# Performance work log

Measured on AMD Instinct MI355X. Metric: run time of the kernel, lower is better.

Reference implementation:

```python
import jax, jax.numpy as jnp
import numpy as np

B, S, D, H = 4, 4096, 1024, 64

def setup_inputs() -> dict:
    key = jax.random.key(0)
    k1, k2, k3, k4 = jax.random.split(key, 4)
    inp = {
        'input': jax.random.normal(k1, (B, S, D), dtype=jnp.float32),
        'Wq': jax.random.normal(k2, (D, H), dtype=jnp.float32) * (D ** -0.5),
        'Wk': jax.random.normal(k3, (D, H), dtype=jnp.float32) * (D ** -0.5),
        'Wv': jax.random.normal(k4, (D, H), dtype=jnp.float32) * (D ** -0.5),
    }
    return inp

def reference(input, Wq, Wk, Wv):
    # Projections: [B,S,D] @ [D,H] -> [B,S,H]
    q = input @ Wq
    k = input @ Wk
    v = input @ Wv
    head_size = Wq.shape[-1]
    # Scaled scores: [B,S,S]
    scores = jnp.einsum('bqh,bkh->bqk', q, k) * (head_size ** -0.5)
    seq_len = input.shape[1]
    causal = jnp.tril(jnp.ones((seq_len, seq_len), dtype=bool))
    masked = jnp.where(causal, scores, -jnp.inf)
    weights = jax.nn.softmax(masked, axis=-1)
    # dropout p=0.0 -> identity
    return jnp.einsum('bqk,bkh->bqh', weights, v)
```

## Files before the change

kernel.cpp:

```cpp
#include <hip/hip_runtime.h>

#define NS 8

typedef __attribute__((ext_vector_type(8))) short sh8;
typedef __attribute__((ext_vector_type(4))) short sh4;
typedef __attribute__((ext_vector_type(4))) float f4;

#define QSCALE 0.18033688011112042f

typedef const __attribute__((address_space(1))) unsigned int* gas_t;
typedef __attribute__((address_space(3))) unsigned int* las_t;
#define GLD16(g, l) __builtin_amdgcn_global_load_lds((gas_t)(g), (las_t)(l), 16, 0, 0)

static __device__ __forceinline__ unsigned short f2bf(float f) {
  unsigned u = __builtin_bit_cast(unsigned, f);
  u += 0x7fffu + ((u >> 16) & 1u);
  return (unsigned short)(u >> 16);
}
static __device__ __forceinline__ float bf2f(unsigned short s) {
  unsigned u = ((unsigned)s) << 16;
  return __builtin_bit_cast(float, u);
}

__global__ __launch_bounds__(256) void wt_kernel(const float* __restrict__ Wq,
                                                 const float* __restrict__ Wk,
                                                 const float* __restrict__ Wv,
                                                 unsigned short* __restrict__ Wt) {
  __shared__ float tile[64 * 65];
  int widx = blockIdx.x >> 4, kt = blockIdx.x & 15;
  const float* W = widx == 0 ? Wq : (widx == 1 ? Wk : Wv);
  int t = threadIdx.x;
  {
    int kl = t >> 2, seg = (t & 3) * 16;
    const float* src = W + (size_t)(kt * 64 + kl) * 64 + seg;
#pragma unroll
    for (int j = 0; j < 16; ++j) tile[kl * 65 + seg + j] = src[j];
  }
  __syncthreads();
  {
    int nl = t >> 2, ks = (t & 3) * 16;
    unsigned short* dst = Wt + (size_t)(widx * 64 + nl) * 1024 + kt * 64 + ks;
#pragma unroll
    for (int j = 0; j < 16; ++j) dst[j] = f2bf(tile[(ks + j) * 65 + nl]);
  }
}

__global__ __launch_bounds__(256, 4) void proj_kernel(const float* __restrict__ in,
                                                      const unsigned short* __restrict__ Wt,
                                                      unsigned short* __restrict__ Qg,
                                                      unsigned short* __restrict__ Kg,
                                                      unsigned short* __restrict__ Vtg) {
  __shared__ __align__(16) char lds[32768];
  int t = threadIdx.x;
  int w = t >> 6, lane = t & 63, q = lane >> 4, l15 = lane & 15;
  int m0 = blockIdx.x * 32;

  int mt_s = w >> 1, i_s = w & 1;
  const float* ga = in + (size_t)(m0 + mt_s * 16 + l15) * 1024 + q * 8 + i_s * 4;
  const unsigned short* gb = Wt + (size_t)(w * 48 + l15) * 1024 + q * 8;

  f4 acc[2][3];
  f4 z = {0.f, 0.f, 0.f, 0.f};
#pragma unroll
  for (int mt = 0; mt < 2; ++mt)
#pragma unroll
    for (int nt = 0; nt < 3; ++nt) acc[mt][nt] = z;

#define STAGE(kt, buf)                                                        \
  {                                                                           \
    int k0 = (kt) * 32;                                                       \
    char* base = lds + (buf) * 16384;                                         \
    GLD16(ga + k0, base + w * 1024);                                          \
    GLD16(gb + k0, base + 4096 + (w * 3 + 0) * 1024);                         \
    GLD16(gb + 16384 + k0, base + 4096 + (w * 3 + 1) * 1024);                 \
    GLD16(gb + 32768 + k0, base + 4096 + (w * 3 + 2) * 1024);                 \
  }

  STAGE(0, 0);
  for (int kt = 0; kt < 32; ++kt) {
    int cur = kt & 1;
    __syncthreads();
    if (kt + 1 < 32) STAGE(kt + 1, cur ^ 1);

    const f4* Af = (const f4*)(lds + cur * 16384);
    f4 lo0 = Af[0 * 64 + lane], hi0 = Af[1 * 64 + lane];
    f4 lo1 = Af[2 * 64 + lane], hi1 = Af[3 * 64 + lane];
    sh8 a0, a1;
#pragma unroll
    for (int j = 0; j < 4; ++j) {
      a0[j] = (short)f2bf(lo0[j]); a0[4 + j] = (short)f2bf(hi0[j]);
      a1[j] = (short)f2bf(lo1[j]); a1[4 + j] = (short)f2bf(hi1[j]);
    }
    const sh8* Bf = (const sh8*)(lds + cur * 16384 + 4096);
#pragma unroll
    for (int nt = 0; nt < 3; ++nt) {
      sh8 bf = Bf[(w * 3 + nt) * 64 + lane];
      acc[0][nt] = __builtin_amdgcn_mfma_f32_16x16x32_bf16(a0, bf, acc[0][nt], 0, 0, 0);
      acc[1][nt] = __builtin_amdgcn_mfma_f32_16x16x32_bf16(a1, bf, acc[1][nt], 0, 0, 0);
    }
  }
#undef STAGE

  float* vred = (float*)lds;
#pragma unroll
  for (int nt = 0; nt < 3; ++nt) {
    int band = w * 3 + nt;
#pragma unroll
    for (int mt = 0; mt < 2; ++mt)
#pragma unroll
      for (int r = 0; r < 4; ++r) {
        int row = mt * 16 + q * 4 + r;
        float v = acc[mt][nt][r];
        if (band < 4) {
          Qg[(size_t)(m0 + row) * 64 + band * 16 + l15] = f2bf(v * QSCALE);
        } else if (band < 8) {
          Kg[(size_t)(m0 + row) * 64 + (band - 4) * 16 + l15] = f2bf(v);
        } else {
          vred[row * 69 + (band - 8) * 16 + l15] = v;
        }
      }
  }
  __syncthreads();
  {
    int h = t >> 2, sl = (t & 3) * 8;
    int bb = m0 >> 12, s0 = m0 & 4095;
    sh8 vv;
#pragma unroll
    for (int j = 0; j < 8; ++j) vv[j] = (short)f2bf(vred[(sl + j) * 69 + h]);
    *(sh8*)&Vtg[(((size_t)(bb * 64 + h)) << 12) + s0 + sl] = vv;
  }
}

__global__ __launch_bounds__(256, 4) void attn_split(const unsigned short* __restrict__ Qg,
                                                     const unsigned short* __restrict__ Kg,
                                                     const unsigned short* __restrict__ Vtg,
                                                     unsigned short* __restrict__ Opart,
                                                     float* __restrict__ Lpart) {
  __shared__ unsigned short Ks[64 * 72];
  __shared__ unsigned short Vs[64 * 72];
  __shared__ unsigned short Pw[4 * 16 * 72];
  int t = threadIdx.x;
  int b = blockIdx.y;
  int qt = 63 - (int)(blockIdx.x >> 3);
  int sp = blockIdx.x & 7;
  int wave = t >> 6, lane = t & 63, quad = lane >> 4, l15 = lane & 15;
  unsigned short* Pws = Pw + wave * 16 * 72;

  int qrow0 = qt * 64 + wave * 16;
  size_t pbase = ((size_t)sp * 4 + b) * 4096;

  int nkt = qt + 1;
  int chunk = (nkt + NS - 1) / NS;
  int t0 = sp * chunk, t1 = min(nkt, t0 + chunk);
  if (t0 >= t1) {
#pragma unroll
    for (int r = 0; r < 4; ++r) {
      size_t row = pbase + qrow0 + quad * 4 + r;
#pragma unroll
      for (int ht = 0; ht < 4; ++ht) Opart[row * 64 + ht * 16 + l15] = 0;
      if (l15 == 0) Lpart[row] = 0.f;
    }
    return;
  }

  sh8 qa[2];
#pragma unroll
  for (int ks = 0; ks < 2; ++ks)
    qa[ks] = *(const sh8*)&Qg[(size_t)((b << 12) + qrow0 + l15) * 64 + ks * 32 + quad * 8];

  sh8 ones;
#pragma unroll
  for (int j = 0; j < 8; ++j) ones[j] = (short)0x3F80;

  f4 o[5];
  f4 z = {0.f, 0.f, 0.f, 0.f};
#pragma unroll
  for (int ht = 0; ht < 5; ++ht) o[ht] = z;

  int r0 = t >> 3, o0 = (t & 7) * 8;
  int r1 = (t + 256) >> 3, o1 = ((t + 256) & 7) * 8;
  const unsigned short* kg0 = Kg + (size_t)((b << 12) + r0) * 64 + o0;
  const unsigned short* kg1 = Kg + (size_t)((b << 12) + r1) * 64 + o1;
  const unsigned short* vg0 = Vtg + (((size_t)(b * 64 + r0)) << 12) + o0;
  const unsigned short* vg1 = Vtg + (((size_t)(b * 64 + r1)) << 12) + o1;

  sh8 kr0, kr1, vr0, vr1;
  {
    size_t ko = (size_t)t0 * 64 * 64;
    kr0 = *(const sh8*)(kg0 + ko); kr1 = *(const sh8*)(kg1 + ko);
    vr0 = *(const sh8*)(vg0 + t0 * 64); vr1 = *(const sh8*)(vg1 + t0 * 64);
  }

  for (int kt = t0; kt < t1; ++kt) {
    __syncthreads();
    *(sh8*)&Ks[r0 * 72 + o0] = kr0;
    *(sh8*)&Ks[r1 * 72 + o1] = kr1;
    *(sh8*)&Vs[r0 * 72 + o0] = vr0;
    *(sh8*)&Vs[r1 * 72 + o1] = vr1;
    if (kt + 1 < t1) {
      size_t ko = (size_t)(kt + 1) * 64 * 64;
      kr0 = *(const sh8*)(kg0 + ko); kr1 = *(const sh8*)(kg1 + ko);
      vr0 = *(const sh8*)(vg0 + (kt + 1) * 64); vr1 = *(const sh8*)(vg1 + (kt + 1) * 64);
    }
    __syncthreads();

    f4 st[4];
#pragma unroll
    for (int nt = 0; nt < 4; ++nt) st[nt] = z;
#pragma unroll
    for (int ks = 0; ks < 2; ++ks) {
#pragma unroll
      for (int nt = 0; nt < 4; ++nt) {
        sh8 kb = *(const sh8*)&Ks[(nt * 16 + l15) * 72 + ks * 32 + quad * 8];
        st[nt] = __builtin_amdgcn_mfma_f32_16x16x32_bf16(kb, qa[ks], st[nt], 0, 0, 0);
      }
    }

    if (kt == nkt - 1) {
      int qrow = qrow0 + l15;
#pragma unroll
      for (int nt = 0; nt < 4; ++nt) {
        int key0 = kt * 64 + nt * 16 + quad * 4;
#pragma unroll
        for (int r = 0; r < 4; ++r)
          if (key0 + r > qrow) st[nt][r] = -__builtin_inff();
      }
    }

#pragma unroll
    for (int nt = 0; nt < 4; ++nt) {
      sh4 pk;
#pragma unroll
      for (int r = 0; r < 4; ++r) pk[r] = (short)f2bf(exp2f(st[nt][r]));
      *(sh4*)&Pws[l15 * 72 + nt * 16 + quad * 4] = pk;
    }
    asm volatile("s_waitcnt lgkmcnt(0)" ::: "memory");

#pragma unroll
    for (int ks = 0; ks < 2; ++ks) {
      sh8 pa = *(const sh8*)&Pws[l15 * 72 + ks * 32 + quad * 8];
#pragma unroll
      for (int ht = 0; ht < 4; ++ht) {
        sh8 vb = *(const sh8*)&Vs[(ht * 16 + l15) * 72 + ks * 32 + quad * 8];
        o[ht] = __builtin_amdgcn_mfma_f32_16x16x32_bf16(pa, vb, o[ht], 0, 0, 0);
      }
      o[4] = __builtin_amdgcn_mfma_f32_16x16x32_bf16(pa, ones, o[4], 0, 0, 0);
    }
  }

#pragma unroll
  for (int r = 0; r < 4; ++r) {
    size_t row = pbase + qrow0 + quad * 4 + r;
#pragma unroll
    for (int ht = 0; ht < 4; ++ht)
      Opart[row * 64 + ht * 16 + l15] = f2bf(o[ht][r]);
    if (l15 == 0) Lpart[row] = o[4][r];
  }
}

__global__ __launch_bounds__(256) void attn_combine(const unsigned short* __restrict__ Opart,
                                                    const float* __restrict__ Lpart,
                                                    float* __restrict__ out) {
  int t = threadIdx.x;
  int rg = blockIdx.x * 4 + (t >> 6);
  int lane = t & 63;
  float acc = 0.f, L = 0.f;
#pragma unroll
  for (int s = 0; s < NS; ++s) {
    L += Lpart[(size_t)s * 16384 + rg];
    acc += bf2f(Opart[((size_t)s * 16384 + rg) * 64 + lane]);
  }
  out[(size_t)rg * 64 + lane] = acc / L;
}

extern "C" void kernel_launch(void* const* d_in, const int* in_sizes, int n_in,
                              void* d_out, int out_size, void* d_ws, size_t ws_size,
                              hipStream_t stream) {
  const float* in = (const float*)d_in[0];
  const float* Wq = (const float*)d_in[1];
  const float* Wk = (const float*)d_in[2];
  const float* Wv = (const float*)d_in[3];
  float* out = (float*)d_out;

  char* ws = (char*)d_ws;
  unsigned short* Wt    = (unsigned short*)ws;
  unsigned short* Qg    = (unsigned short*)(ws + 393216);
  unsigned short* Kg    = (unsigned short*)(ws + 2490368);
  unsigned short* Vtg   = (unsigned short*)(ws + 4587520);
  unsigned short* Opart = (unsigned short*)(ws + 6684672);
  float*          Lpart = (float*)(ws + 23461888);

  hipLaunchKernelGGL(wt_kernel, dim3(48), dim3(256), 0, stream, Wq, Wk, Wv, Wt);
  hipLaunchKernelGGL(proj_kernel, dim3(512), dim3(256), 0, stream, in, Wt, Qg, Kg, Vtg);
  hipLaunchKernelGGL(attn_split, dim3(64 * NS, 4), dim3(256), 0, stream,
                     Qg, Kg, Vtg, Opart, Lpart);
  hipLaunchKernelGGL(attn_combine, dim3(4096), dim3(256), 0, stream,
                     Opart, Lpart, out);
}
```

Measured before the change: 158.7 us.

## Pre-swizzle weights into MFMA fragment layout and drop LDS staging in projection

The weight-transpose kernel now writes bf16 weights directly in the per-lane MFMA B-fragment order. The projection kernel therefore reads A and B straight from global memory into registers, with no LDS double buffering or barriers. It also halves the rows per block to 16, doubling the grid to 1024 blocks. V is written transposed directly from the accumulators as 4-element vectors instead of going through an LDS transpose. The aim is to remove LDS traffic, synchronisation and the V reduction pass. The cost is that each wave now loads the input A tile redundantly, A reads are less coalesced, and latency hiding relies on unrolling and occupancy.

```diff
diff --git a/kernel.cpp b/kernel.cpp
--- a/kernel.cpp
+++ b/kernel.cpp
@@ -7,10 +7,6 @@
 typedef __attribute__((ext_vector_type(4))) float f4;
 
 #define QSCALE 0.18033688011112042f
-
-typedef const __attribute__((address_space(1))) unsigned int* gas_t;
-typedef __attribute__((address_space(3))) unsigned int* las_t;
-#define GLD16(g, l) __builtin_amdgcn_global_load_lds((gas_t)(g), (las_t)(l), 16, 0, 0)
 
 static __device__ __forceinline__ unsigned short f2bf(float f) {
   unsigned u = __builtin_bit_cast(unsigned, f);
@@ -25,109 +21,75 @@
 __global__ __launch_bounds__(256) void wt_kernel(const float* __restrict__ Wq,
                                                  const float* __restrict__ Wk,
                                                  const float* __restrict__ Wv,
-                                                 unsigned short* __restrict__ Wt) {
-  __shared__ float tile[64 * 65];
-  int widx = blockIdx.x >> 4, kt = blockIdx.x & 15;
+                                                 unsigned short* __restrict__ Wt2) {
+  int blk = blockIdx.x;
+  int band = blk >> 3;
+  int widx = band >> 2;
   const float* W = widx == 0 ? Wq : (widx == 1 ? Wk : Wv);
-  int t = threadIdx.x;
-  {
-    int kl = t >> 2, seg = (t & 3) * 16;
-    const float* src = W + (size_t)(kt * 64 + kl) * 64 + seg;
-#pragma unroll
-    for (int j = 0; j < 16; ++j) tile[kl * 65 + seg + j] = src[j];
-  }
-  __syncthreads();
-  {
-    int nl = t >> 2, ks = (t & 3) * 16;
-    unsigned short* dst = Wt + (size_t)(widx * 64 + nl) * 1024 + kt * 64 + ks;
-#pragma unroll
-    for (int j = 0; j < 16; ++j) dst[j] = f2bf(tile[(ks + j) * 65 + nl]);
-  }
+  int ncol = (band & 3) * 16;
+  int t = threadIdx.x;
+  int kt = (blk & 7) * 4 + (t >> 6);
+  int lane = t & 63, q = lane >> 4, l15 = lane & 15;
+  const float* src = W + (size_t)(kt * 32 + q * 8) * 64 + ncol + l15;
+  sh8 o;
+#pragma unroll
+  for (int j = 0; j < 8; ++j) o[j] = (short)f2bf(src[(size_t)j * 64]);
+  *(sh8*)&Wt2[((size_t)(band * 32 + kt) * 64 + lane) * 8] = o;
 }
 
 __global__ __launch_bounds__(256, 4) void proj_kernel(const float* __restrict__ in,
-                                                      const unsigned short* __restrict__ Wt,
+                                                      const unsigned short* __restrict__ Wt2,
                                                       unsigned short* __restrict__ Qg,
                                                       unsigned short* __restrict__ Kg,
                                                       unsigned short* __restrict__ Vtg) {
-  __shared__ __align__(16) char lds[32768];
   int t = threadIdx.x;
   int w = t >> 6, lane = t & 63, q = lane >> 4, l15 = lane & 15;
-  int m0 = blockIdx.x * 32;
-
-  int mt_s = w >> 1, i_s = w & 1;
-  const float* ga = in + (size_t)(m0 + mt_s * 16 + l15) * 1024 + q * 8 + i_s * 4;
-  const unsigned short* gb = Wt + (size_t)(w * 48 + l15) * 1024 + q * 8;
-
-  f4 acc[2][3];
+  int m0 = blockIdx.x * 16;
+
+  const float* arow = in + (size_t)(m0 + l15) * 1024 + q * 8;
+  const unsigned short* bbase = Wt2 + (size_t)(w * 3) * 16384 + lane * 8;
+
+  f4 acc[3];
   f4 z = {0.f, 0.f, 0.f, 0.f};
 #pragma unroll
-  for (int mt = 0; mt < 2; ++mt)
-#pragma unroll
-    for (int nt = 0; nt < 3; ++nt) acc[mt][nt] = z;
-
-#define STAGE(kt, buf)                                                        \
-  {                                                                           \
-    int k0 = (kt) * 32;                                                       \
-    char* base = lds + (buf) * 16384;                                         \
-    GLD16(ga + k0, base + w * 1024);                                          \
-    GLD16(gb + k0, base + 4096 + (w * 3 + 0) * 1024);                         \
-    GLD16(gb + 16384 + k0, base + 4096 + (w * 3 + 1) * 1024);                 \
-    GLD16(gb + 32768 + k0, base + 4096 + (w * 3 + 2) * 1024);                 \
-  }
-
-  STAGE(0, 0);
+  for (int nt = 0; nt < 3; ++nt) acc[nt] = z;
+
+#pragma unroll 4
   for (int kt = 0; kt < 32; ++kt) {
-    int cur = kt & 1;
-    __syncthreads();
-    if (kt + 1 < 32) STAGE(kt + 1, cur ^ 1);
-
-    const f4* Af = (const f4*)(lds + cur * 16384);
-    f4 lo0 = Af[0 * 64 + lane], hi0 = Af[1 * 64 + lane];
-    f4 lo1 = Af[2 * 64 + lane], hi1 = Af[3 * 64 + lane];
-    sh8 a0, a1;
+    f4 lo = *(const f4*)(arow + kt * 32);
+    f4 hi = *(const f4*)(arow + kt * 32 + 4);
+    sh8 a;
 #pragma unroll
     for (int j = 0; j < 4; ++j) {
-      a0[j] = (short)f2bf(lo0[j]); a0[4 + j] = (short)f2bf(hi0[j]);
-      a1[j] = (short)f2bf(lo1[j]); a1[4 + j] = (short)f2bf(hi1[j]);
-    }
-    const sh8* Bf = (const sh8*)(lds + cur * 16384 + 4096);
+      a[j] = (short)f2bf(lo[j]);
+      a[4 + j] = (short)f2bf(hi[j]);
+    }
 #pragma unroll
     for (int nt = 0; nt < 3; ++nt) {
-      sh8 bf = Bf[(w * 3 + nt) * 64 + lane];
-      acc[0][nt] = __builtin_amdgcn_mfma_f32_16x16x32_bf16(a0, bf, acc[0][nt], 0, 0, 0);
-      acc[1][nt] = __builtin_amdgcn_mfma_f32_16x16x32_bf16(a1, bf, acc[1][nt], 0, 0, 0);
-    }
-  }
-#undef STAGE
-
-  float* vred = (float*)lds;
+      sh8 bf = *(const sh8*)(bbase + nt * 16384 + kt * 512);
+      acc[nt] = __builtin_amdgcn_mfma_f32_16x16x32_bf16(a, bf, acc[nt], 0, 0, 0);
+    }
+  }
+
+  int bb = m0 >> 12, s0 = m0 & 4095;
 #pragma unroll
   for (int nt = 0; nt < 3; ++nt) {
     int band = w * 3 + nt;
-#pragma unroll
-    for (int mt = 0; mt < 2; ++mt)
-#pragma unroll
-      for (int r = 0; r < 4; ++r) {
-        int row = mt * 16 + q * 4 + r;
-        float v = acc[mt][nt][r];
-        if (band < 4) {
-          Qg[(size_t)(m0 + row) * 64 + band * 16 + l15] = f2bf(v * QSCALE);
-        } else if (band < 8) {
-          Kg[(size_t)(m0 + row) * 64 + (band - 4) * 16 + l15] = f2bf(v);
-        } else {
-          vred[row * 69 + (band - 8) * 16 + l15] = v;
-        }
-      }
-  }
-  __syncthreads();
-  {
-    int h = t >> 2, sl = (t & 3) * 8;
-    int bb = m0 >> 12, s0 = m0 & 4095;
-    sh8 vv;
-#pragma unroll
-    for (int j = 0; j < 8; ++j) vv[j] = (short)f2bf(vred[(sl + j) * 69 + h]);
-    *(sh8*)&Vtg[(((size_t)(bb * 64 + h)) << 12) + s0 + sl] = vv;
+    if (band < 4) {
+#pragma unroll
+      for (int r = 0; r < 4; ++r)
+        Qg[(size_t)(m0 + q * 4 + r) * 64 + band * 16 + l15] = f2bf(acc[nt][r] * QSCALE);
+    } else if (band < 8) {
+#pragma unroll
+      for (int r = 0; r < 4; ++r)
+        Kg[(size_t)(m0 + q * 4 + r) * 64 + (band - 4) * 16 + l15] = f2bf(acc[nt][r]);
+    } else {
+      int h = (band - 8) * 16 + l15;
+      sh4 pv;
+#pragma unroll
+      for (int r = 0; r < 4; ++r) pv[r] = (short)f2bf(acc[nt][r]);
+      *(sh4*)&Vtg[(((size_t)(bb * 64 + h)) << 12) + s0 + q * 4] = pv;
+    }
   }
 }
 
@@ -283,15 +245,15 @@
   float* out = (float*)d_out;
 
   char* ws = (char*)d_ws;
-  unsigned short* Wt    = (unsigned short*)ws;
+  unsigned short* Wt2   = (unsigned short*)ws;
   unsigned short* Qg    = (unsigned short*)(ws + 393216);
   unsigned short* Kg    = (unsigned short*)(ws + 2490368);
   unsigned short* Vtg   = (unsigned short*)(ws + 4587520);
   unsigned short* Opart = (unsigned short*)(ws + 6684672);
   float*          Lpart = (float*)(ws + 23461888);
 
-  hipLaunchKernelGGL(wt_kernel, dim3(48), dim3(256), 0, stream, Wq, Wk, Wv, Wt);
-  hipLaunchKernelGGL(proj_kernel, dim3(512), dim3(256), 0, stream, in, Wt, Qg, Kg, Vtg);
+  hipLaunchKernelGGL(wt_kernel, dim3(96), dim3(256), 0, stream, Wq, Wk, Wv, Wt2);
+  hipLaunchKernelGGL(proj_kernel, dim3(1024), dim3(256), 0, stream, in, Wt2, Qg, Kg, Vtg);
   hipLaunchKernelGGL(attn_split, dim3(64 * NS, 4), dim3(256), 0, stream,
                      Qg, Kg, Vtg, Opart, Lpart);
   hipLaunchKernelGGL(attn_combine, dim3(4096), dim3(256), 0, stream,
```

After: 164.9 us. 3.9% more time.
